# Kernel optimization log

Measured on AMD Instinct MI355X. Metric: run time of the kernel, lower is better.

Reference implementation:

```python
import jax, jax.numpy as jnp
import numpy as np

N_NODES = 15000
N_EDGES = 60000
D_NODE_IN = 74
D_EDGE_IN = 12
D = 64            # node_out_feats
D_EHID = 128      # edge_hidden_feats
N_STEPS = 6
BN_EPS = 1e-5


def setup_inputs() -> dict:
    key = jax.random.key(0)
    ks = jax.random.split(key, 16)
    def lin(k, fan_in, shape):
        return jax.random.normal(k, shape, jnp.float32) / np.sqrt(fan_in)
    inp = {
        "node_feats": jax.random.normal(ks[0], (N_NODES, D_NODE_IN), jnp.float32),
        "edge_feats": jax.random.normal(ks[1], (N_EDGES, D_EDGE_IN), jnp.float32),
        "src": jax.random.randint(ks[2], (N_EDGES,), 0, N_NODES, jnp.int32),
        "dst": jax.random.randint(ks[3], (N_EDGES,), 0, N_NODES, jnp.int32),
        # project_node_feats: Linear(node_in, D)
        "W_proj": lin(ks[4], D_NODE_IN, (D_NODE_IN, D)),
        "b_proj": jnp.zeros((D,), jnp.float32),
        # edge network: Linear(edge_in, ehid) -> ReLU -> Linear(ehid, D*D)
        "W_e1": lin(ks[5], D_EDGE_IN, (D_EDGE_IN, D_EHID)),
        "b_e1": jnp.zeros((D_EHID,), jnp.float32),
        "W_e2": lin(ks[6], D_EHID, (D_EHID, D * D)),
        "b_e2": jnp.zeros((D * D,), jnp.float32),
        # NNConv bias + BatchNorm affine params
        "conv_bias": jnp.zeros((D,), jnp.float32),
        "bn_gamma": jnp.ones((D,), jnp.float32),
        "bn_beta": jnp.zeros((D,), jnp.float32),
        # GRU (single layer): torch layout W_ih [3D, D], W_hh [3D, D]
        "W_ih": lin(ks[7], D, (3 * D, D)),
        "W_hh": lin(ks[8], D, (3 * D, D)),
        "b_ih": jnp.zeros((3 * D,), jnp.float32),
        "b_hh": jnp.zeros((3 * D,), jnp.float32),
    }
    return inp


def reference(node_feats, edge_feats, W_proj, b_proj, W_e1, b_e1, W_e2, b_e2,
              conv_bias, bn_gamma, bn_beta, W_ih, W_hh, b_ih, b_hh, src, dst):
    n_nodes = node_feats.shape[0]

    # project_node_feats: Linear + ReLU
    h = jax.nn.relu(node_feats @ W_proj + b_proj)          # [N, D]
    hidden = h                                              # GRU hidden state

    # edge MLP is a pure function of static edge_feats -> compute once
    ew = jax.nn.relu(edge_feats @ W_e1 + b_e1) @ W_e2 + b_e2
    ew = ew.reshape(-1, D, D)                               # [E, D, D]

    # mean-aggregation normalizer (DGL mean: 0 for isolated nodes)
    deg = jax.ops.segment_sum(jnp.ones_like(dst, jnp.float32), dst,
                              num_segments=n_nodes)
    inv_deg = jnp.where(deg > 0, 1.0 / jnp.maximum(deg, 1.0), 0.0)[:, None]

    for _ in range(N_STEPS):
        # per-edge matvec message: (h_src^T W_e); sum over d_in commutes
        # with the mean reduction, so reduce vectors instead of matrices.
        msg = jnp.einsum('ei,eio->eo', h[src], ew)          # [E, D]
        rst = jax.ops.segment_sum(msg, dst, num_segments=n_nodes) * inv_deg
        rst = rst + conv_bias
        # BatchNorm1d (training mode: batch statistics, biased variance)
        mu = rst.mean(axis=0)
        var = rst.var(axis=0)
        rst = (rst - mu) * jax.lax.rsqrt(var + BN_EPS) * bn_gamma + bn_beta
        m = jax.nn.relu(rst)
        # GRU cell (torch gate order: r, z, n)
        gi = m @ W_ih.T + b_ih
        gh = hidden @ W_hh.T + b_hh
        i_r, i_z, i_n = jnp.split(gi, 3, axis=-1)
        h_r, h_z, h_n = jnp.split(gh, 3, axis=-1)
        r = jax.nn.sigmoid(i_r + h_r)
        z = jax.nn.sigmoid(i_z + h_z)
        n = jnp.tanh(i_n + r * h_n)
        hidden = (1.0 - z) * n + z * hidden
        h = hidden
    return h
```

## Files before the change

kernel.cpp:

```cpp
#include <hip/hip_runtime.h>
#include <math.h>

#define NN 15000
#define NE 60000
#define DIN 74
#define DEIN 12
#define DD 64
#define EH 128
#define NG 8192
#define NSTEPS 6
#define NRB 235
#define KAB 384
#define NTMAX 18752
#define NFB 586

typedef unsigned short ushort_t;
typedef __attribute__((ext_vector_type(8))) short short8v;
typedef __attribute__((ext_vector_type(4))) float float4v;

__device__ __forceinline__ float bsf(unsigned short u){
  union { unsigned int i; float f; } v; v.i = ((unsigned int)u) << 16; return v.f;
}
__device__ __forceinline__ unsigned short fsb(float f){
  union { float f; unsigned int i; } v; v.f = f;
  unsigned int x = v.i;
  return (unsigned short)((x + 0x7FFFu + ((x >> 16) & 1u)) >> 16);
}

__global__ void k_sniff(const ushort_t* __restrict__ nf16,
                        const int* __restrict__ dsti, int* __restrict__ flags){
  __shared__ int cnt[2];
  int t = threadIdx.x;
  if (t < 2) cnt[t] = 0;
  __syncthreads();
  int bad = 0;
  for (int i = t; i < 1024; i += 256){
    unsigned short u = nf16[2*i];
    int e = (u >> 7) & 0xFF;
    if (e < 96 || e > 159) bad++;
  }
  if (bad) atomicAdd(&cnt[0], bad);
  if (t < 256 && dsti[2*t+1] == 0) atomicAdd(&cnt[1], 1);
  __syncthreads();
  if (t == 0){
    flags[0] = (cnt[0] > 300) ? 1 : 0;
    flags[1] = (cnt[1] > 250) ? 1 : 0;
  }
}

struct CanonArgs {
  const void* in[15];
  float* out[15];
  int n[15];
};
__global__ void k_canon_all(CanonArgs a, const int* __restrict__ flags){
  int j = blockIdx.y;
  int n = a.n[j];
  int fp32 = flags[0];
  const void* in = a.in[j];
  float* out = a.out[j];
  for (int i = blockIdx.x*256 + threadIdx.x; i < n; i += gridDim.x*256){
    if (fp32) out[i] = ((const float*)in)[i];
    else      out[i] = bsf(((const ushort_t*)in)[i]);
  }
}
__global__ void k_canoni(const void* __restrict__ in, int* __restrict__ out,
                         int n, const int* __restrict__ flags){
  int i = blockIdx.x*256 + threadIdx.x;
  if (i >= n) return;
  long long v = flags[1] ? ((const long long*)in)[i]
                         : (long long)((const int*)in)[i];
  int vi = (int)v;
  if (vi < 0) vi = 0;
  if (vi >= NN) vi = NN-1;
  out[i] = vi;
}

__global__ void k_proj(const float* __restrict__ nf, const float* __restrict__ Wp,
                       const float* __restrict__ bp, float* __restrict__ hid,
                       ushort_t* __restrict__ ab){
  __shared__ float nfl[4][DIN];
  int t = threadIdx.x, blk = blockIdx.x;
  for (int idx = t; idx < 4*DIN; idx += 256){
    int vl = idx / DIN, i = idx - vl*DIN;
    nfl[vl][i] = nf[(size_t)(blk*4+vl)*DIN + i];
  }
  __syncthreads();
  int vl = t >> 6, o = t & 63;
  int v = blk*4 + vl;
  float acc = bp[o];
  for (int i = 0; i < DIN; ++i) acc += nfl[vl][i] * Wp[i*DD + o];
  float r = fmaxf(acc, 0.f);
  hid[(size_t)v*DD + o] = r;
  ushort_t hh = fsb(r);
  float hl = r - bsf(hh);
  ab[(size_t)v*KAB + 64 + o]  = hh;
  ab[(size_t)v*KAB + 192 + o] = fsb(hl);
  ab[(size_t)v*KAB + 320 + o] = hh;
}

__global__ void k_emlp(const float* __restrict__ ef, const float* __restrict__ W1,
                       const float* __restrict__ b1, ushort_t* __restrict__ thi,
                       ushort_t* __restrict__ tlo){
  __shared__ float efl[2][DEIN];
  int t = threadIdx.x, blk = blockIdx.x;
  if (t < 2*DEIN){
    int el = t / DEIN, i = t - el*DEIN;
    efl[el][i] = ef[(size_t)(blk*2+el)*DEIN + i];
  }
  __syncthreads();
  int el = t >> 7, c = t & 127;
  float acc = b1[c];
  for (int i = 0; i < DEIN; ++i) acc += efl[el][i] * W1[i*EH + c];
  float tv = fmaxf(acc, 0.f);
  ushort_t hiv = fsb(tv);
  size_t off = (size_t)(blk*2+el)*EH + c;
  thi[off] = hiv;
  tlo[off] = fsb(tv - bsf(hiv));
}
__global__ void k_zpad(ushort_t* __restrict__ thi, ushort_t* __restrict__ tlo){
  int t = threadIdx.x;
  thi[(size_t)NE*EH + t] = 0;
  tlo[(size_t)NE*EH + t] = 0;
}

__global__ void k_w2q(const float* __restrict__ W2, const float* __restrict__ b2,
                      ushort_t* __restrict__ w2q, ushort_t* __restrict__ w2b){
  int idx = blockIdx.x*256 + threadIdx.x;
  if (idx < NG*DD){
    int n = idx >> 6, i = idx & 63;
    int kq = n >> 11, rem = n & 2047;
    int o = rem >> 5, kl = rem & 31;
    int kg = kq*32 + kl;
    w2q[idx] = fsb(W2[(size_t)kg*4096 + i*64 + o]);
  } else if (idx < NG*DD + DD*DD){
    int r = idx - NG*DD;
    int o = r >> 6, i = r & 63;
    w2b[r] = fsb(b2[i*64 + o]);
  }
}

__global__ void k_wgru(const float* __restrict__ Wih, const float* __restrict__ Whh,
                       ushort_t* __restrict__ wg){
  int pos = blockIdx.x*256 + threadIdx.x;
  if (pos >= 256*KAB) return;
  int c = pos / KAB, k = pos - c*KAB;
  int kb = k >> 6, i = k & 63;
  int g = c >> 6, o = c & 63;
  float w = 0.f;
  if ((kb & 1) == 0){
    if (g == 0)      w = Wih[(size_t)(o)*64 + i];
    else if (g == 1) w = Wih[(size_t)(64+o)*64 + i];
    else if (g == 2) w = Wih[(size_t)(128+o)*64 + i];
  } else {
    if (g == 0)      w = Whh[(size_t)(o)*64 + i];
    else if (g == 1) w = Whh[(size_t)(64+o)*64 + i];
    else if (g == 3) w = Whh[(size_t)(128+o)*64 + i];
  }
  ushort_t hi = fsb(w);
  wg[pos] = (kb >= 4) ? fsb(w - bsf(hi)) : hi;
}

__global__ void k_zero(int* __restrict__ p, int n){
  int i = blockIdx.x*256 + threadIdx.x;
  if (i < n) p[i] = 0;
}
__global__ void k_deg(const int* __restrict__ idxarr, int* __restrict__ deg){
  int e = blockIdx.x*256 + threadIdx.x;
  if (e < NE) atomicAdd(&deg[idxarr[e]], 1);
}
__global__ void k_scan(const int* __restrict__ deg, int* __restrict__ rowp,
                       float* __restrict__ invd){
  __shared__ int ssum[256];
  int t = threadIdx.x;
  const int STRIP = (NN + 255) / 256;
  int lo = t*STRIP, hi = (lo + STRIP < NN) ? lo + STRIP : NN;
  int s = 0;
  for (int i = lo; i < hi; ++i) s += deg[i];
  ssum[t] = s;
  __syncthreads();
  if (t == 0){
    int acc = 0;
    for (int i = 0; i < 256; ++i){ int v = ssum[i]; ssum[i] = acc; acc += v; }
  }
  __syncthreads();
  int acc = ssum[t];
  for (int i = lo; i < hi; ++i){
    rowp[i] = acc;
    int d = deg[i];
    invd[i] = (d > 0) ? 1.0f/(float)d : 0.0f;
    acc += d;
  }
  if (t == 255) rowp[NN] = acc;
}
__global__ void k_scatter(const int* __restrict__ idxarr, const int* __restrict__ rowp,
                          int* __restrict__ cursor, int* __restrict__ eidx){
  int e = blockIdx.x*256 + threadIdx.x;
  if (e < NE){
    int d = idxarr[e];
    int pos = atomicAdd(&cursor[d], 1);
    eidx[rowp[d] + pos] = e;
  }
}

__global__ void k_tiles(const int* __restrict__ rowp, int* __restrict__ tnode,
                        int* __restrict__ tbase, int* __restrict__ tcnt,
                        int* __restrict__ ntb){
  __shared__ int ss[256];
  int t = threadIdx.x;
  const int STRIP = (NN + 255) / 256;
  int lo = t*STRIP, hi = lo + STRIP; if (hi > NN) hi = NN;
  int c = 0;
  for (int i = lo; i < hi; ++i){
    int deg = rowp[i+1] - rowp[i];
    c += (deg + 15) >> 4;
  }
  ss[t] = c;
  __syncthreads();
  if (t == 0){
    int a = 0;
    for (int i = 0; i < 256; ++i){ int v = ss[i]; ss[i] = a; a += v; }
    ntb[0] = a;
  }
  __syncthreads();
  int pos = ss[t];
  for (int i = lo; i < hi; ++i){
    int b = rowp[i], deg = rowp[i+1] - b;
    for (int r = 0; r < deg; r += 16){
      tnode[pos] = i; tbase[pos] = b + r;
      int c2 = deg - r; tcnt[pos] = (c2 > 16) ? 16 : c2;
      ++pos;
    }
  }
}

__global__ __launch_bounds__(512,4) void k_fused5(
    const ushort_t* __restrict__ ab, const ushort_t* __restrict__ w2q,
    const ushort_t* __restrict__ w2b, const ushort_t* __restrict__ thi,
    const ushort_t* __restrict__ tlo,
    const int* __restrict__ tnode, const int* __restrict__ tbase,
    const int* __restrict__ tcnt, const int* __restrict__ ntb,
    const int* __restrict__ eidx, float* __restrict__ msg){
  __shared__ __align__(16) ushort_t Gl[32768];
  __shared__ float bhl[32*66];
  __shared__ int nodl[32], cntl[32], basel[32];
  __shared__ int eidl[32][16];

  int tid = threadIdx.x;
  int nt = ntb[0];
  int T0 = blockIdx.x * 32;
  if (T0 >= nt) return;
  int wv = tid >> 6, lane = tid & 63;
  int lr = lane & 15, quad = lane >> 4;

  if (tid < 32){
    int gt = T0 + tid;
    int node = 0, base = 0, cnt = 0;
    if (gt < nt){ node = tnode[gt]; base = tbase[gt]; cnt = tcnt[gt]; }
    nodl[tid] = node; basel[tid] = base; cntl[tid] = cnt;
  }
  __syncthreads();
  {
    int j = tid >> 4, sl = tid & 15;
    int eid = NE;
    if (sl < cntl[j]) eid = eidx[basel[j] + sl];
    eidl[j][sl] = eid;
  }
  short8v hf0k0, hf0k1, hf1k0, hf1k1;
  {
    int n0 = nodl[lr], n1 = nodl[16 + lr];
    hf0k0 = *(const short8v*)(ab + (size_t)n0*KAB + 64 + quad*8);
    hf0k1 = *(const short8v*)(ab + (size_t)n0*KAB + 96 + quad*8);
    hf1k0 = *(const short8v*)(ab + (size_t)n1*KAB + 64 + quad*8);
    hf1k1 = *(const short8v*)(ab + (size_t)n1*KAB + 96 + quad*8);
  }
  {
    int ot = wv & 3, mh = wv >> 2;
    float4v ba = (float4v){0.f,0.f,0.f,0.f};
    short8v a0 = *(const short8v*)(w2b + (size_t)(ot*16 + lr)*DD + quad*8);
    short8v a1 = *(const short8v*)(w2b + (size_t)(ot*16 + lr)*DD + 32 + quad*8);
    ba = __builtin_amdgcn_mfma_f32_16x16x32_bf16(a0, mh ? hf1k0 : hf0k0, ba, 0,0,0);
    ba = __builtin_amdgcn_mfma_f32_16x16x32_bf16(a1, mh ? hf1k1 : hf0k1, ba, 0,0,0);
    #pragma unroll
    for (int reg = 0; reg < 4; ++reg)
      bhl[(mh*16 + lr)*66 + ot*16 + quad*4 + reg] = ba[reg];
  }

  int j0 = wv*4;
  for (int oh = 0; oh < 2; ++oh){
    float4v acc[4][2];
    #pragma unroll
    for (int j = 0; j < 4; ++j)
      #pragma unroll
      for (int ot = 0; ot < 2; ++ot)
        acc[j][ot] = (float4v){0.f,0.f,0.f,0.f};
    for (int kq = 0; kq < 4; ++kq){
      __syncthreads();
      #pragma unroll 2
      for (int it = 0; it < 8; ++it){
        int tile = wv*8 + it;
        int nrow = kq*2048 + oh*1024 + tile*16 + lr;
        const ushort_t* arow = w2q + (size_t)nrow*DD;
        short8v a0 = *(const short8v*)(arow + quad*8);
        short8v a1 = *(const short8v*)(arow + 32 + quad*8);
        int ol = tile >> 1;
        int klb = ((tile & 1) << 4) + quad*4;
        int q8 = klb >> 3, jj = klb & 7;
        #pragma unroll
        for (int mh = 0; mh < 2; ++mh){
          float4v g = (float4v){0.f,0.f,0.f,0.f};
          g = __builtin_amdgcn_mfma_f32_16x16x32_bf16(a0, mh ? hf1k0 : hf0k0, g, 0,0,0);
          g = __builtin_amdgcn_mfma_f32_16x16x32_bf16(a1, mh ? hf1k1 : hf0k1, g, 0,0,0);
          int m = mh*16 + lr;
          unsigned int p0 = (unsigned int)fsb(g[0]) | ((unsigned int)fsb(g[1]) << 16);
          unsigned int p1 = (unsigned int)fsb(g[2]) | ((unsigned int)fsb(g[3]) << 16);
          int byt = ((((m*4 + q8)*32 + ol) << 4) + jj*2) ^ ((m & 7) << 4);
          uint2 pv; pv.x = p0; pv.y = p1;
          *(uint2*)((char*)Gl + byt) = pv;
        }
      }
      __syncthreads();
      short8v th0, th1, th2, th3, tw0, tw1, tw2, tw3;
      {
        size_t kqo = (size_t)kq*32 + quad*8;
        int e0 = eidl[j0+0][lr], e1 = eidl[j0+1][lr];
        int e2 = eidl[j0+2][lr], e3 = eidl[j0+3][lr];
        th0 = *(const short8v*)(thi + (size_t)e0*EH + kqo);
        tw0 = *(const short8v*)(tlo + (size_t)e0*EH + kqo);
        th1 = *(const short8v*)(thi + (size_t)e1*EH + kqo);
        tw1 = *(const short8v*)(tlo + (size_t)e1*EH + kqo);
        th2 = *(const short8v*)(thi + (size_t)e2*EH + kqo);
        tw2 = *(const short8v*)(tlo + (size_t)e2*EH + kqo);
        th3 = *(const short8v*)(thi + (size_t)e3*EH + kqo);
        tw3 = *(const short8v*)(tlo + (size_t)e3*EH + kqo);
      }
      #pragma unroll
      for (int j = 0; j < 4; ++j){
        int m = j0 + j;
        int swz = (m & 7) << 4;
        short8v thj = (j==0)?th0:(j==1)?th1:(j==2)?th2:th3;
        short8v twj = (j==0)?tw0:(j==1)?tw1:(j==2)?tw2:tw3;
        #pragma unroll
        for (int ot = 0; ot < 2; ++ot){
          int byt = (((m*4 + quad)*32 + ot*16 + lr) << 4) ^ swz;
          short8v gf = *(const short8v*)((const char*)Gl + byt);
          acc[j][ot] = __builtin_amdgcn_mfma_f32_16x16x32_bf16(thj, gf, acc[j][ot], 0,0,0);
          acc[j][ot] = __builtin_amdgcn_mfma_f32_16x16x32_bf16(twj, gf, acc[j][ot], 0,0,0);
        }
      }
    }
    #pragma unroll
    for (int j = 0; j < 4; ++j){
      int m = j0 + j;
      #pragma unroll
      for (int ot = 0; ot < 2; ++ot){
        int o = oh*32 + ot*16 + lr;
        float bb = bhl[m*66 + o];
        #pragma unroll
        for (int reg = 0; reg < 4; ++reg){
          int eid = eidl[m][quad*4 + reg];
          if (eid < NE) msg[(size_t)eid*DD + o] = acc[j][ot][reg] + bb;
        }
      }
    }
  }
}

__global__ void k_red(const float* __restrict__ msg, const int* __restrict__ rowp_d,
                      const int* __restrict__ eidx_d, const float* __restrict__ invd,
                      const float* __restrict__ cbias, float* __restrict__ rst,
                      float* __restrict__ part){
  __shared__ float ls[256], ls2[256];
  int t = threadIdx.x, blk = blockIdx.x;
  int o = t & 63, gg = t >> 6;
  float cb = cbias[o];
  float s = 0.f, s2 = 0.f;
  #pragma unroll 1
  for (int j = 0; j < 16; ++j){
    int n = blk*64 + gg*16 + j;
    if (n >= NN) break;
    int b = rowp_d[n], e = rowp_d[n+1];
    float a0 = 0.f, a1 = 0.f, a2 = 0.f, a3 = 0.f;
    int i = b;
    for (; i + 3 < e; i += 4){
      int e0 = eidx_d[i], e1 = eidx_d[i+1], e2 = eidx_d[i+2], e3 = eidx_d[i+3];
      a0 += msg[(size_t)e0*DD + o];
      a1 += msg[(size_t)e1*DD + o];
      a2 += msg[(size_t)e2*DD + o];
      a3 += msg[(size_t)e3*DD + o];
    }
    for (; i < e; ++i) a0 += msg[(size_t)eidx_d[i]*DD + o];
    float x = ((a0 + a1) + (a2 + a3)) * invd[n] + cb;
    rst[(size_t)n*DD + o] = x;
    s += x; s2 += x*x;
  }
  ls[t] = s; ls2[t] = s2;
  __syncthreads();
  if (gg == 0){
    part[blk*128 + o]      = ls[o] + ls[64+o] + ls[128+o] + ls[192+o];
    part[blk*128 + 64 + o] = ls2[o] + ls2[64+o] + ls2[128+o] + ls2[192+o];
  }
}

__global__ void k_bnf(const float* __restrict__ part, float* __restrict__ stats){
  __shared__ float sh[128];
  int t = threadIdx.x;
  float s0 = 0.f, s1 = 0.f, s2 = 0.f, s3 = 0.f;
  int b = 0;
  for (; b + 3 < NRB; b += 4){
    s0 += part[b*128 + t];
    s1 += part[(b+1)*128 + t];
    s2 += part[(b+2)*128 + t];
    s3 += part[(b+3)*128 + t];
  }
  for (; b < NRB; ++b) s0 += part[b*128 + t];
  sh[t] = (s0 + s1) + (s2 + s3);
  __syncthreads();
  if (t < 64){
    float mu = sh[t] / (float)NN;
    float var = sh[64+t] / (float)NN - mu*mu;
    if (var < 0.f) var = 0.f;
    stats[t] = mu;
    stats[64 + t] = rsqrtf(var + 1e-5f);
  }
}

__global__ void k_gru_pre(const float* __restrict__ rst, const float* __restrict__ stats,
      const float* __restrict__ gamma, const float* __restrict__ beta,
      ushort_t* __restrict__ ab){
  int t = threadIdx.x, blk = blockIdx.x;
  int vl = t >> 6, o = t & 63;
  int v = blk*4 + vl;
  float x = rst[(size_t)v*DD + o];
  float m = fmaxf((x - stats[o])*stats[64+o]*gamma[o] + beta[o], 0.f);
  ushort_t mh = fsb(m);
  float mlo = m - bsf(mh);
  ab[(size_t)v*KAB + o]       = mh;
  ab[(size_t)v*KAB + 128 + o] = fsb(mlo);
  ab[(size_t)v*KAB + 256 + o] = mh;
}

__global__ __launch_bounds__(256) void k_gru_gemm(const ushort_t* __restrict__ ab,
        const ushort_t* __restrict__ wg, float* __restrict__ gbuf){
  __shared__ __align__(16) ushort_t As[128][136];
  __shared__ __align__(16) ushort_t Bs[64][136];
  int t = threadIdx.x;
  int n0 = blockIdx.x * 64;
  int m0 = blockIdx.y * 128;
  int w = t >> 6, lane = t & 63;
  int lrow = lane & 15, quad = lane >> 4;
  float4v acc[2][4];
  #pragma unroll
  for (int mt = 0; mt < 2; ++mt)
    #pragma unroll
    for (int nt = 0; nt < 4; ++nt) acc[mt][nt] = (float4v){0.f,0.f,0.f,0.f};
  for (int kt = 0; kt < 3; ++kt){
    __syncthreads();
    #pragma unroll
    for (int it = 0; it < 8; ++it){
      int cid = t + it*256;
      int r = cid >> 4, ko = (cid & 15) * 8;
      int gm = m0 + r; if (gm >= NN) gm = NN-1;
      *(uint4*)&As[r][ko] = *(const uint4*)(ab + (size_t)gm*KAB + kt*128 + ko);
    }
    #pragma unroll
    for (int it = 0; it < 4; ++it){
      int cid = t + it*256;
      int r = cid >> 4, ko = (cid & 15) * 8;
      *(uint4*)&Bs[r][ko] = *(const uint4*)(wg + (size_t)(n0 + r)*KAB + kt*128 + ko);
    }
    __syncthreads();
    #pragma unroll
    for (int ks = 0; ks < 4; ++ks){
      short8v a0 = *(const short8v*)&As[w*32 + lrow][ks*32 + quad*8];
      short8v a1 = *(const short8v*)&As[w*32 + 16 + lrow][ks*32 + quad*8];
      #pragma unroll
      for (int nt = 0; nt < 4; ++nt){
        short8v b = *(const short8v*)&Bs[nt*16 + lrow][ks*32 + quad*8];
        acc[0][nt] = __builtin_amdgcn_mfma_f32_16x16x32_bf16(a0, b, acc[0][nt], 0, 0, 0);
        acc[1][nt] = __builtin_amdgcn_mfma_f32_16x16x32_bf16(a1, b, acc[1][nt], 0, 0, 0);
      }
    }
  }
  #pragma unroll
  for (int mt = 0; mt < 2; ++mt){
    #pragma unroll
    for (int nt = 0; nt < 4; ++nt){
      int col = n0 + nt*16 + lrow;
      #pragma unroll
      for (int reg = 0; reg < 4; ++reg){
        int m = m0 + w*32 + mt*16 + quad*4 + reg;
        if (m < NN) gbuf[(size_t)m*256 + col] = acc[mt][nt][reg];
      }
    }
  }
}

__global__ void k_gru_fin(const float* __restrict__ gbuf,
      const float* __restrict__ bih, const float* __restrict__ bhh,
      float* __restrict__ hid, ushort_t* __restrict__ ab,
      float* __restrict__ out, int write_out){
  int t = threadIdx.x, blk = blockIdx.x;
  int vl = t >> 6, o = t & 63;
  int v = blk*4 + vl;
  const float* gb = gbuf + (size_t)v*256;
  float aR  = gb[o]       + bih[o]      + bhh[o];
  float aZ  = gb[64 + o]  + bih[64+o]   + bhh[64+o];
  float aNi = gb[128 + o] + bih[128+o];
  float aNh = gb[192 + o] + bhh[128+o];
  float hprev = hid[(size_t)v*DD + o];
  float r = 1.f/(1.f+__expf(-aR));
  float z = 1.f/(1.f+__expf(-aZ));
  float n = tanhf(aNi + r*aNh);
  float hnew = (1.f - z)*n + z*hprev;
  hid[(size_t)v*DD + o] = hnew;
  ushort_t hh = fsb(hnew);
  float hl = hnew - bsf(hh);
  ab[(size_t)v*KAB + 64 + o]  = hh;
  ab[(size_t)v*KAB + 192 + o] = fsb(hl);
  ab[(size_t)v*KAB + 320 + o] = hh;
  if (write_out) out[(size_t)v*DD + o] = hnew;
}

extern "C" void kernel_launch(void* const* d_in, const int* in_sizes, int n_in,
                              void* d_out, int out_size, void* d_ws, size_t ws_size,
                              hipStream_t stream){
  (void)out_size; (void)ws_size;
  float* out = (float*)d_out;

  int p_nf=-1,p_ef=-1,p_src=-1,p_dst=-1,p_Wp=-1,p_bp=-1,p_W1=-1,p_b1=-1,
      p_W2=-1,p_b2=-1,p_cb=-1,p_gam=-1,p_bet=-1,p_Wih=-1,p_Whh=-1,p_bih=-1,p_bhh=-1;
  int c60000=0,c64=0,c12288=0,c192=0;
  for (int i = 0; i < n_in; ++i){
    switch (in_sizes[i]){
      case 1110000: p_nf = i; break;
      case 720000:  p_ef = i; break;
      case 60000:   if (c60000++ == 0) p_src = i; else p_dst = i; break;
      case 4736:    p_Wp = i; break;
      case 64:      { if (c64==0) p_bp=i; else if (c64==1) p_cb=i;
                      else if (c64==2) p_gam=i; else p_bet=i; c64++; } break;
      case 1536:    p_W1 = i; break;
      case 128:     p_b1 = i; break;
      case 524288:  p_W2 = i; break;
      case 4096:    p_b2 = i; break;
      case 12288:   if (c12288++ == 0) p_Wih = i; else p_Whh = i; break;
      case 192:    if (c192++ == 0) p_bih = i; else p_bhh = i; break;
      default: break;
    }
  }

  char* p = (char*)d_ws;
  auto alloc = [&](size_t bytes)->char*{
    char* r = p; p += (bytes + 255) & ~(size_t)255; return r;
  };
  int* flags = (int*)alloc(256);
  const int FPOS[15] = {p_nf,p_ef,p_Wp,p_bp,p_W1,p_b1,p_W2,p_b2,p_cb,p_gam,p_bet,
                        p_Wih,p_Whh,p_bih,p_bhh};
  CanonArgs ca;
  int maxn = 0;
  for (int j = 0; j < 15; ++j){
    int n = in_sizes[FPOS[j]];
    ca.in[j]  = d_in[FPOS[j]];
    ca.out[j] = (float*)alloc((size_t)n * 4);
    ca.n[j]   = n;
    if (n > maxn) maxn = n;
  }
  const float* nf  = ca.out[0];  const float* ef  = ca.out[1];
  const float* Wp  = ca.out[2];  const float* bp  = ca.out[3];
  const float* W1  = ca.out[4];  const float* b1  = ca.out[5];
  const float* W2  = ca.out[6];  const float* b2  = ca.out[7];
  const float* cb  = ca.out[8];  const float* gam = ca.out[9];
  const float* bet = ca.out[10]; const float* Wih = ca.out[11];
  const float* Whh = ca.out[12]; const float* bih = ca.out[13];
  const float* bhh = ca.out[14];
  int* srcc = (int*)alloc((size_t)NE*4);
  int* dstc = (int*)alloc((size_t)NE*4);

  ushort_t* thi   = (ushort_t*)alloc((size_t)(NE+1)*EH*2);
  ushort_t* tlo   = (ushort_t*)alloc((size_t)(NE+1)*EH*2);
  ushort_t* w2q   = (ushort_t*)alloc((size_t)NG*DD*2);
  ushort_t* w2b   = (ushort_t*)alloc((size_t)DD*DD*2);
  float* hid      = (float*)alloc((size_t)NN*DD*4);
  ushort_t* ab    = (ushort_t*)alloc((size_t)NN*KAB*2);
  ushort_t* wg    = (ushort_t*)alloc((size_t)256*KAB*2);
  float* gbuf     = (float*)alloc((size_t)NN*256*4);
  float* rst      = (float*)alloc((size_t)NN*DD*4);
  float* msg      = (float*)alloc((size_t)NE*DD*4);
  float* part     = (float*)alloc((size_t)NRB*128*4);
  float* stats    = (float*)alloc(128*4);
  int* degall     = (int*)alloc((size_t)4*NN*4);
  int* deg  = degall;
  int* curd = degall + NN;
  int* deg2 = degall + 2*NN; int* cursor2 = degall + 3*NN;
  float* invd = (float*)alloc((size_t)NN*4);
  int* rowp_d = (int*)alloc((size_t)(NN+1)*4);
  int* eidx_d = (int*)alloc((size_t)NE*4);
  int* rowp2  = (int*)alloc((size_t)(NN+1)*4);
  float* invd2= (float*)alloc((size_t)NN*4);
  int* eidx2  = (int*)alloc((size_t)NE*4);
  int* tnode  = (int*)alloc((size_t)NTMAX*4);
  int* tbase  = (int*)alloc((size_t)NTMAX*4);
  int* tcnt   = (int*)alloc((size_t)NTMAX*4);
  int* ntb    = (int*)alloc(256);

  k_sniff<<<1, 256, 0, stream>>>((const ushort_t*)d_in[p_nf], (const int*)d_in[p_dst], flags);
  k_canon_all<<<dim3((maxn+255)/256, 15), 256, 0, stream>>>(ca, flags);
  k_canoni<<<(NE+255)/256, 256, 0, stream>>>(d_in[p_src], srcc, NE, flags);
  k_canoni<<<(NE+255)/256, 256, 0, stream>>>(d_in[p_dst], dstc, NE, flags);

  k_proj <<<NN/4,  256, 0, stream>>>(nf, Wp, bp, hid, ab);
  k_emlp <<<NE/2,  256, 0, stream>>>(ef, W1, b1, thi, tlo);
  k_zpad <<<1, 128, 0, stream>>>(thi, tlo);
  k_w2q  <<<(NG*DD + DD*DD + 255)/256, 256, 0, stream>>>(W2, b2, w2q, w2b);
  k_wgru <<<(256*KAB+255)/256, 256, 0, stream>>>(Wih, Whh, wg);
  k_zero <<<(4*NN+255)/256, 256, 0, stream>>>(degall, 4*NN);
  k_deg  <<<(NE+255)/256, 256, 0, stream>>>(dstc, deg);
  k_deg  <<<(NE+255)/256, 256, 0, stream>>>(srcc, deg2);
  k_scan <<<1, 256, 0, stream>>>(deg,  rowp_d, invd);
  k_scan <<<1, 256, 0, stream>>>(deg2, rowp2, invd2);
  k_scatter<<<(NE+255)/256, 256, 0, stream>>>(dstc, rowp_d, curd, eidx_d);
  k_scatter<<<(NE+255)/256, 256, 0, stream>>>(srcc, rowp2, cursor2, eidx2);
  k_tiles<<<1, 256, 0, stream>>>(rowp2, tnode, tbase, tcnt, ntb);

  for (int s = 0; s < NSTEPS; ++s){
    k_fused5<<<NFB, 512, 0, stream>>>(ab, w2q, w2b, thi, tlo,
                                      tnode, tbase, tcnt, ntb, eidx2, msg);
    k_red <<<NRB, 256, 0, stream>>>(msg, rowp_d, eidx_d, invd, cb, rst, part);
    k_bnf <<<1, 128, 0, stream>>>(part, stats);
    k_gru_pre <<<NN/4, 256, 0, stream>>>(rst, stats, gam, bet, ab);
    k_gru_gemm<<<dim3(4, (NN+127)/128), 256, 0, stream>>>(ab, wg, gbuf);
    k_gru_fin <<<NN/4, 256, 0, stream>>>(gbuf, bih, bhh, hid, ab, out,
                                         (s == NSTEPS-1) ? 1 : 0);
  }
}
```

Baseline: 1.129 ms.

## Write messages in dst-sorted order, fuse BN stats into reduction, hoist edge loads

The fused message kernel now writes each edge message to its destination-sorted slot (via a precomputed epos map), so the reduction kernel reads contiguous rows instead of gathering through eidx. The BatchNorm finalisation kernel is folded into the reduction using a last-block atomic counter, which removes one launch per step. Edge-feature loads are moved ahead of the G-tile computation so their latency overlaps the MFMA work, and bf16 packing switches to the hip intrinsic. The costs are an extra epos lookup, scattered stores in the message kernel, and a threadfence plus atomic per reduction block.

```diff
diff --git a/kernel.cpp b/kernel.cpp
--- a/kernel.cpp
+++ b/kernel.cpp
@@ -1,4 +1,5 @@
 #include <hip/hip_runtime.h>
+#include <hip/hip_bf16.h>
 #include <math.h>
 
 #define NN 15000
@@ -25,6 +26,10 @@
   union { float f; unsigned int i; } v; v.f = f;
   unsigned int x = v.i;
   return (unsigned short)((x + 0x7FFFu + ((x >> 16) & 1u)) >> 16);
+}
+__device__ __forceinline__ unsigned int pkbf(float a, float b){
+  __hip_bfloat162 r = __float22bfloat162_rn(make_float2(a, b));
+  union { __hip_bfloat162 h; unsigned int u; } v; v.h = r; return v.u;
 }
 
 __global__ void k_sniff(const ushort_t* __restrict__ nf16,
@@ -194,12 +199,15 @@
   if (t == 255) rowp[NN] = acc;
 }
 __global__ void k_scatter(const int* __restrict__ idxarr, const int* __restrict__ rowp,
-                          int* __restrict__ cursor, int* __restrict__ eidx){
+                          int* __restrict__ cursor, int* __restrict__ eidx,
+                          int* __restrict__ epos){
   int e = blockIdx.x*256 + threadIdx.x;
   if (e < NE){
     int d = idxarr[e];
     int pos = atomicAdd(&cursor[d], 1);
-    eidx[rowp[d] + pos] = e;
+    int slot = rowp[d] + pos;
+    eidx[slot] = e;
+    if (epos) epos[e] = slot;
   }
 }
 
@@ -234,17 +242,19 @@
   }
 }
 
-__global__ __launch_bounds__(512,4) void k_fused5(
+__global__ __launch_bounds__(512,4) void k_fused6(
     const ushort_t* __restrict__ ab, const ushort_t* __restrict__ w2q,
     const ushort_t* __restrict__ w2b, const ushort_t* __restrict__ thi,
     const ushort_t* __restrict__ tlo,
     const int* __restrict__ tnode, const int* __restrict__ tbase,
     const int* __restrict__ tcnt, const int* __restrict__ ntb,
-    const int* __restrict__ eidx, float* __restrict__ msg){
+    const int* __restrict__ eidx, const int* __restrict__ epos,
+    float* __restrict__ msg){
   __shared__ __align__(16) ushort_t Gl[32768];
   __shared__ float bhl[32*66];
   __shared__ int nodl[32], cntl[32], basel[32];
   __shared__ int eidl[32][16];
+  __shared__ int posl[32][16];
 
   int tid = threadIdx.x;
   int nt = ntb[0];
@@ -262,9 +272,13 @@
   __syncthreads();
   {
     int j = tid >> 4, sl = tid & 15;
-    int eid = NE;
-    if (sl < cntl[j]) eid = eidx[basel[j] + sl];
+    int eid = NE, ps = 0;
+    if (sl < cntl[j]){
+      eid = eidx[basel[j] + sl];
+      ps = epos[eid];
+    }
     eidl[j][sl] = eid;
+    posl[j][sl] = ps;
   }
   short8v hf0k0, hf0k1, hf1k0, hf1k1;
   {
@@ -296,6 +310,20 @@
         acc[j][ot] = (float4v){0.f,0.f,0.f,0.f};
     for (int kq = 0; kq < 4; ++kq){
       __syncthreads();
+      short8v th0, th1, th2, th3, tw0, tw1, tw2, tw3;
+      {
+        size_t kqo = (size_t)kq*32 + quad*8;
+        int e0 = eidl[j0+0][lr], e1 = eidl[j0+1][lr];
+        int e2 = eidl[j0+2][lr], e3 = eidl[j0+3][lr];
+        th0 = *(const short8v*)(thi + (size_t)e0*EH + kqo);
+        tw0 = *(const short8v*)(tlo + (size_t)e0*EH + kqo);
+        th1 = *(const short8v*)(thi + (size_t)e1*EH + kqo);
+        tw1 = *(const short8v*)(tlo + (size_t)e1*EH + kqo);
+        th2 = *(const short8v*)(thi + (size_t)e2*EH + kqo);
+        tw2 = *(const short8v*)(tlo + (size_t)e2*EH + kqo);
+        th3 = *(const short8v*)(thi + (size_t)e3*EH + kqo);
+        tw3 = *(const short8v*)(tlo + (size_t)e3*EH + kqo);
+      }
       #pragma unroll 2
       for (int it = 0; it < 8; ++it){
         int tile = wv*8 + it;
@@ -312,28 +340,14 @@
           g = __builtin_amdgcn_mfma_f32_16x16x32_bf16(a0, mh ? hf1k0 : hf0k0, g, 0,0,0);
           g = __builtin_amdgcn_mfma_f32_16x16x32_bf16(a1, mh ? hf1k1 : hf0k1, g, 0,0,0);
           int m = mh*16 + lr;
-          unsigned int p0 = (unsigned int)fsb(g[0]) | ((unsigned int)fsb(g[1]) << 16);
-          unsigned int p1 = (unsigned int)fsb(g[2]) | ((unsigned int)fsb(g[3]) << 16);
+          unsigned int p0 = pkbf(g[0], g[1]);
+          unsigned int p1 = pkbf(g[2], g[3]);
           int byt = ((((m*4 + q8)*32 + ol) << 4) + jj*2) ^ ((m & 7) << 4);
           uint2 pv; pv.x = p0; pv.y = p1;
           *(uint2*)((char*)Gl + byt) = pv;
         }
       }
       __syncthreads();
-      short8v th0, th1, th2, th3, tw0, tw1, tw2, tw3;
-      {
-        size_t kqo = (size_t)kq*32 + quad*8;
-        int e0 = eidl[j0+0][lr], e1 = eidl[j0+1][lr];
-        int e2 = eidl[j0+2][lr], e3 = eidl[j0+3][lr];
-        th0 = *(const short8v*)(thi + (size_t)e0*EH + kqo);
-        tw0 = *(const short8v*)(tlo + (size_t)e0*EH + kqo);
-        th1 = *(const short8v*)(thi + (size_t)e1*EH + kqo);
-        tw1 = *(const short8v*)(tlo + (size_t)e1*EH + kqo);
-        th2 = *(const short8v*)(thi + (size_t)e2*EH + kqo);
-        tw2 = *(const short8v*)(tlo + (size_t)e2*EH + kqo);
-        th3 = *(const short8v*)(thi + (size_t)e3*EH + kqo);
-        tw3 = *(const short8v*)(tlo + (size_t)e3*EH + kqo);
-      }
       #pragma unroll
       for (int j = 0; j < 4; ++j){
         int m = j0 + j;
@@ -358,8 +372,9 @@
         float bb = bhl[m*66 + o];
         #pragma unroll
         for (int reg = 0; reg < 4; ++reg){
-          int eid = eidl[m][quad*4 + reg];
-          if (eid < NE) msg[(size_t)eid*DD + o] = acc[j][ot][reg] + bb;
+          int sl = quad*4 + reg;
+          int eid = eidl[m][sl];
+          if (eid < NE) msg[(size_t)posl[m][sl]*DD + o] = acc[j][ot][reg] + bb;
         }
       }
     }
@@ -367,10 +382,11 @@
 }
 
 __global__ void k_red(const float* __restrict__ msg, const int* __restrict__ rowp_d,
-                      const int* __restrict__ eidx_d, const float* __restrict__ invd,
-                      const float* __restrict__ cbias, float* __restrict__ rst,
-                      float* __restrict__ part){
+                      const float* __restrict__ invd, const float* __restrict__ cbias,
+                      float* __restrict__ rst, float* __restrict__ part,
+                      int* __restrict__ cnt, float* __restrict__ stats){
   __shared__ float ls[256], ls2[256];
+  __shared__ int lastflag;
   int t = threadIdx.x, blk = blockIdx.x;
   int o = t & 63, gg = t >> 6;
   float cb = cbias[o];
@@ -383,13 +399,12 @@
     float a0 = 0.f, a1 = 0.f, a2 = 0.f, a3 = 0.f;
     int i = b;
     for (; i + 3 < e; i += 4){
-      int e0 = eidx_d[i], e1 = eidx_d[i+1], e2 = eidx_d[i+2], e3 = eidx_d[i+3];
-      a0 += msg[(size_t)e0*DD + o];
-      a1 += msg[(size_t)e1*DD + o];
-      a2 += msg[(size_t)e2*DD + o];
-      a3 += msg[(size_t)e3*DD + o];
-    }
-    for (; i < e; ++i) a0 += msg[(size_t)eidx_d[i]*DD + o];
+      a0 += msg[(size_t)i*DD + o];
+      a1 += msg[(size_t)(i+1)*DD + o];
+      a2 += msg[(size_t)(i+2)*DD + o];
+      a3 += msg[(size_t)(i+3)*DD + o];
+    }
+    for (; i < e; ++i) a0 += msg[(size_t)i*DD + o];
     float x = ((a0 + a1) + (a2 + a3)) * invd[n] + cb;
     rst[(size_t)n*DD + o] = x;
     s += x; s2 += x*x;
@@ -400,28 +415,31 @@
     part[blk*128 + o]      = ls[o] + ls[64+o] + ls[128+o] + ls[192+o];
     part[blk*128 + 64 + o] = ls2[o] + ls2[64+o] + ls2[128+o] + ls2[192+o];
   }
-}
-
-__global__ void k_bnf(const float* __restrict__ part, float* __restrict__ stats){
-  __shared__ float sh[128];
-  int t = threadIdx.x;
-  float s0 = 0.f, s1 = 0.f, s2 = 0.f, s3 = 0.f;
-  int b = 0;
-  for (; b + 3 < NRB; b += 4){
-    s0 += part[b*128 + t];
-    s1 += part[(b+1)*128 + t];
-    s2 += part[(b+2)*128 + t];
-    s3 += part[(b+3)*128 + t];
-  }
-  for (; b < NRB; ++b) s0 += part[b*128 + t];
-  sh[t] = (s0 + s1) + (s2 + s3);
-  __syncthreads();
-  if (t < 64){
-    float mu = sh[t] / (float)NN;
-    float var = sh[64+t] / (float)NN - mu*mu;
-    if (var < 0.f) var = 0.f;
-    stats[t] = mu;
-    stats[64 + t] = rsqrtf(var + 1e-5f);
+  __threadfence();
+  __syncthreads();
+  if (t == 0) lastflag = (atomicAdd(cnt, 1) == NRB - 1) ? 1 : 0;
+  __syncthreads();
+  if (lastflag){
+    if (t < 128){
+      float s0 = 0.f, s1 = 0.f, s2b = 0.f, s3 = 0.f;
+      int b = 0;
+      for (; b + 3 < NRB; b += 4){
+        s0  += part[b*128 + t];
+        s1  += part[(b+1)*128 + t];
+        s2b += part[(b+2)*128 + t];
+        s3  += part[(b+3)*128 + t];
+      }
+      for (; b < NRB; ++b) s0 += part[b*128 + t];
+      ls[t] = (s0 + s1) + (s2b + s3);
+    }
+    __syncthreads();
+    if (t < 64){
+      float mu = ls[t] / (float)NN;
+      float var = ls[64+t] / (float)NN - mu*mu;
+      if (var < 0.f) var = 0.f;
+      stats[t] = mu;
+      stats[64 + t] = rsqrtf(var + 1e-5f);
+    }
   }
 }
 
@@ -595,6 +613,7 @@
   float* invd = (float*)alloc((size_t)NN*4);
   int* rowp_d = (int*)alloc((size_t)(NN+1)*4);
   int* eidx_d = (int*)alloc((size_t)NE*4);
+  int* epos   = (int*)alloc((size_t)NE*4);
   int* rowp2  = (int*)alloc((size_t)(NN+1)*4);
   float* invd2= (float*)alloc((size_t)NN*4);
   int* eidx2  = (int*)alloc((size_t)NE*4);
@@ -602,6 +621,7 @@
   int* tbase  = (int*)alloc((size_t)NTMAX*4);
   int* tcnt   = (int*)alloc((size_t)NTMAX*4);
   int* ntb    = (int*)alloc(256);
+  int* cnts   = (int*)alloc(256);
 
   k_sniff<<<1, 256, 0, stream>>>((const ushort_t*)d_in[p_nf], (const int*)d_in[p_dst], flags);
   k_canon_all<<<dim3((maxn+255)/256, 15), 256, 0, stream>>>(ca, flags);
@@ -614,19 +634,20 @@
   k_w2q  <<<(NG*DD + DD*DD + 255)/256, 256, 0, stream>>>(W2, b2, w2q, w2b);
   k_wgru <<<(256*KAB+255)/256, 256, 0, stream>>>(Wih, Whh, wg);
   k_zero <<<(4*NN+255)/256, 256, 0, stream>>>(degall, 4*NN);
+  k_zero <<<1, 64, 0, stream>>>(cnts, 64);
   k_deg  <<<(NE+255)/256, 256, 0, stream>>>(dstc, deg);
   k_deg  <<<(NE+255)/256, 256, 0, stream>>>(srcc, deg2);
   k_scan <<<1, 256, 0, stream>>>(deg,  rowp_d, invd);
   k_scan <<<1, 256, 0, stream>>>(deg2, rowp2, invd2);
-  k_scatter<<<(NE+255)/256, 256, 0, stream>>>(dstc, rowp_d, curd, eidx_d);
-  k_scatter<<<(NE+255)/256, 256, 0, stream>>>(srcc, rowp2, cursor2, eidx2);
+  k_scatter<<<(NE+255)/256, 256, 0, stream>>>(dstc, rowp_d, curd, eidx_d, epos);
+  k_scatter<<<(NE+255)/256, 256, 0, stream>>>(srcc, rowp2, cursor2, eidx2, (int*)0);
   k_tiles<<<1, 256, 0, stream>>>(rowp2, tnode, tbase, tcnt, ntb);
 
   for (int s = 0; s < NSTEPS; ++s){
-    k_fused5<<<NFB, 512, 0, stream>>>(ab, w2q, w2b, thi, tlo,
-                                      tnode, tbase, tcnt, ntb, eidx2, msg);
-    k_red <<<NRB, 256, 0, stream>>>(msg, rowp_d, eidx_d, invd, cb, rst, part);
-    k_bnf <<<1, 128, 0, stream>>>(part, stats);
+    k_fused6<<<NFB, 512, 0, stream>>>(ab, w2q, w2b, thi, tlo,
+                                      tnode, tbase, tcnt, ntb, eidx2, epos, msg);
+    k_red <<<NRB, 256, 0, stream>>>(msg, rowp_d, invd, cb, rst, part,
+                                    cnts + s, stats);
     k_gru_pre <<<NN/4, 256, 0, stream>>>(rst, stats, gam, bet, ab);
     k_gru_gemm<<<dim3(4, (NN+127)/128), 256, 0, stream>>>(ab, wg, gbuf);
     k_gru_fin <<<NN/4, 256, 0, stream>>>(gbuf, bih, bhh, hid, ab, out,
```

New measurement: 1.162 ms. 1.03x slower.
